# Performance work log

Hardware: AMD Instinct MI355X
Metric: run time of the kernel (lower is better)

The kernel has to match this reference:

```python
import jax, jax.numpy as jnp
import numpy as np

D = 120000   # sample_size
H1 = 600     # sample_size/200
H2 = 300     # sample_size/400
H3 = 200     # sample_size/600
DENSITY = 0.1  # sparselinear default connectivity
B = 512
EPS = 1e-5

_LAYER_SPECS = [(H1, D), (H1, H1), (H2, H1), (H3, H2), (H3, H3)]


def _make_idx(key, out_d, in_d, nnz):
    k1, k2 = jax.random.split(key)
    rows = jax.random.randint(k1, (nnz,), 0, out_d)
    cols = jax.random.randint(k2, (nnz,), 0, in_d)
    return jnp.stack([rows, cols]).astype(jnp.int32)


def setup_inputs() -> dict:
    key = jax.random.key(0)
    ks = jax.random.split(key, 32)
    inp = {"x": jax.random.normal(ks[0], (B, D), jnp.float32)}
    for i, (o, ii) in enumerate(_LAYER_SPECS, 1):
        nnz = int(DENSITY * o * ii)
        scale = 1.0 / np.sqrt(DENSITY * ii)  # kaiming-like fan-in scaling on nonzeros
        inp[f"idx{i}"] = _make_idx(ks[3 * i], o, ii, nnz)
        inp[f"val{i}"] = jax.random.normal(ks[3 * i + 1], (nnz,), jnp.float32) * scale
        inp[f"b{i}"] = jnp.zeros((o,), jnp.float32)
    for j, d in enumerate([H1, H2, H3], 1):
        inp[f"g{j}"] = jnp.ones((d,), jnp.float32)
        inp[f"be{j}"] = jnp.zeros((d,), jnp.float32)
    return inp


def _sp_linear(x, idx, vals, bias, out_d):
    # COO sparse linear: y = x @ W^T + b, W scattered from (row, col, val)
    in_d = x.shape[1]
    W = jnp.zeros((out_d, in_d), x.dtype).at[idx[0], idx[1]].add(vals)
    return x @ W.T + bias


def _bn(x, g, b):
    # BatchNorm1d, training mode: biased batch variance
    m = x.mean(axis=0)
    v = x.var(axis=0)
    return (x - m) * jax.lax.rsqrt(v + EPS) * g + b


def reference(x, idx1, val1, b1, idx2, val2, b2, idx3, val3, b3,
              idx4, val4, b4, idx5, val5, b5,
              g1, be1, g2, be2, g3, be3):
    h = jax.nn.silu(_bn(_sp_linear(x, idx1, val1, b1, H1), g1, be1))
    h = jax.nn.silu(_sp_linear(h, idx2, val2, b2, H1))
    h = jax.nn.silu(_bn(_sp_linear(h, idx3, val3, b3, H2), g2, be2))
    h = jax.nn.silu(_bn(_sp_linear(h, idx4, val4, b4, H3), g3, be3))
    return _sp_linear(h, idx5, val5, b5, H3)
```

## Files before the change

### kernel.cpp

```cpp
#include <hip/hip_runtime.h>

typedef unsigned short ushort_t;
typedef unsigned int uint_t;

typedef __bf16 bf16x8 __attribute__((ext_vector_type(8)));
typedef float  floatx4 __attribute__((ext_vector_type(4)));

#define AS3 __attribute__((address_space(3)))
#define AS1 __attribute__((address_space(1)))

#define BATCH 512
#define D_IN  120000
#define N1P   640
#define N2P   640
#define N3P   320
#define N4P   256
#define N5P   256

#define HALF    60000
#define CHW     15000
#define NREG    1200
#define NB      256
#define RSTRIDE 6912

static constexpr long O_W1 = 0;
static constexpr long SZ_W1 = 640L * 120000 * 2;
static constexpr long O_W2 = O_W1 + SZ_W1;
static constexpr long SZ_W2 = 640L * 640 * 4;
static constexpr long O_W3 = O_W2 + SZ_W2;
static constexpr long SZ_W3 = 320L * 640 * 4;
static constexpr long O_W4 = O_W3 + SZ_W3;
static constexpr long SZ_W4 = 256L * 320 * 4;
static constexpr long O_W5 = O_W4 + SZ_W4;
static constexpr long SZ_W5 = 256L * 256 * 4;
static constexpr long O_Y1 = O_W5 + SZ_W5;
static constexpr long SZ_Y1 = 512L * 640 * 4;
static constexpr long ZERO_OFF = O_W2;
static constexpr long ZERO_BYTES = (O_Y1 + SZ_Y1) - O_W2;
static constexpr long O_XB = O_Y1 + SZ_Y1;
static constexpr long SZ_XB = 512L * 120000 * 2;
static constexpr long O_CNT = O_XB;
static constexpr long O_OFF = O_CNT + (long)NREG * NB * 4;
static constexpr long O_TOT = O_OFF + (long)NB * NREG * 4;
static constexpr long O_REC = O_TOT + 4800;
static constexpr long O_H1 = O_XB;
static constexpr long O_H2 = O_H1 + 512L * 640 * 4;
static constexpr long O_Y3 = O_H2 + 512L * 640 * 4;
static constexpr long O_H3 = O_Y3 + 512L * 320 * 4;
static constexpr long O_Y4 = O_H3 + 512L * 320 * 4;
static constexpr long O_H4 = O_Y4 + 512L * 256 * 4;

__device__ __forceinline__ ushort_t f2bf(float f) {
    union { float f; uint_t u; } x;
    x.f = f;
    uint_t u = x.u;
    return (ushort_t)((u + 0x7FFFu + ((u >> 16) & 1u)) >> 16);
}
__device__ __forceinline__ float silu_f(float z) {
    return z / (1.f + expf(-z));
}
__device__ __forceinline__ void load16_lds(const void* g, void* l) {
    __builtin_amdgcn_global_load_lds((const AS1 char*)g, (AS3 char*)l, 16, 0, 0);
}

__global__ void zero_f4(float4* __restrict__ p, long n4) {
    long stride = (long)gridDim.x * blockDim.x;
    for (long i = (long)blockIdx.x * blockDim.x + threadIdx.x; i < n4; i += stride)
        p[i] = make_float4(0.f, 0.f, 0.f, 0.f);
}

__global__ void cast_f32_bf16(const float* __restrict__ X, ushort_t* __restrict__ Xb, long n8) {
    long t = (long)blockIdx.x * blockDim.x + threadIdx.x;
    if (t >= n8) return;
    const float4* p = (const float4*)X + 2 * t;
    float4 a = p[0], b = p[1];
    union { ushort_t us[8]; uint4 v; } u;
    u.us[0] = f2bf(a.x); u.us[1] = f2bf(a.y); u.us[2] = f2bf(a.z); u.us[3] = f2bf(a.w);
    u.us[4] = f2bf(b.x); u.us[5] = f2bf(b.y); u.us[6] = f2bf(b.z); u.us[7] = f2bf(b.w);
    ((uint4*)Xb)[t] = u.v;
}

__global__ __launch_bounds__(512) void hist1(const int* __restrict__ idx, int nnz, int chunk,
                                             int* __restrict__ counts ) {
    __shared__ uint_t h[NREG];
    const int b = blockIdx.x, t = threadIdx.x;
    for (int i = t; i < NREG; i += 512) h[i] = 0;
    __syncthreads();
    const int s = b * chunk;
    const int e = min(s + chunk, nnz);
    for (int i = s + t; i < e; i += 512) {
        int r = idx[i];
        int c = idx[nnz + i];
        atomicAdd(&h[r * 2 + (c >= HALF ? 1 : 0)], 1u);
    }
    __syncthreads();
    for (int i = t; i < NREG; i += 512) counts[(long)i * NB + b] = (int)h[i];
}

__global__ __launch_bounds__(NB) void scan1(const int* __restrict__ counts ,
                                            int* __restrict__ offs ,
                                            int* __restrict__ totals) {
    __shared__ int s[NB];
    const int reg = blockIdx.x, t = threadIdx.x;
    const int v = counts[(long)reg * NB + t];
    s[t] = v;
    __syncthreads();
    for (int o = 1; o < NB; o <<= 1) {
        int x = (t >= o) ? s[t - o] : 0;
        __syncthreads();
        s[t] += x;
        __syncthreads();
    }
    offs[(long)t * NREG + reg] = s[t] - v;
    if (t == NB - 1) totals[reg] = s[t];
}

__global__ __launch_bounds__(512) void scatter1(const int* __restrict__ idx,
                                                const float* __restrict__ vals,
                                                int nnz, int chunk,
                                                const int* __restrict__ offs ,
                                                int2* __restrict__ rec) {
    __shared__ int cur[NREG];
    const int b = blockIdx.x, t = threadIdx.x;
    const int* ob = offs + (long)b * NREG;
    for (int i = t; i < NREG; i += 512) cur[i] = i * RSTRIDE + ob[i];
    __syncthreads();
    const int s = b * chunk;
    const int e = min(s + chunk, nnz);
    for (int i = s + t; i < e; i += 512) {
        int r = idx[i];
        int c = idx[nnz + i];
        float v = vals[i];
        int h = (c >= HALF) ? 1 : 0;
        int reg = r * 2 + h;
        int slot = atomicAdd(&cur[reg], 1);
        if (slot < (reg + 1) * RSTRIDE)
            rec[slot] = make_int2(c - h * HALF, __float_as_int(v));
    }
}

__global__ __launch_bounds__(512) void build_w1(const int2* __restrict__ rec,
                                                const int* __restrict__ totals,
                                                ushort_t* __restrict__ W) {
    const int bid = blockIdx.x;
    const int r = bid >> 1, h = bid & 1;
    const int t = threadIdx.x;
    ushort_t* dstbase = W + (size_t)r * D_IN + h * HALF;

    if (r >= 600) {
        uint4 z = make_uint4(0, 0, 0, 0);
        for (int j = t * 8; j < HALF; j += 512 * 8) *(uint4*)(dstbase + j) = z;
        return;
    }

    __shared__ int2 lrec[RSTRIDE];
    __shared__ float acc[CHW];

    const int reg = r * 2 + h;
    const int n = min(totals[reg], RSTRIDE);
    const int2* src = rec + (long)reg * RSTRIDE;
    for (int i = t; i < n; i += 512) lrec[i] = src[i];
    __syncthreads();

#pragma unroll
    for (int ch = 0; ch < 4; ch++) {
        for (int j = t * 4; j < CHW; j += 512 * 4)
            *(float4*)&acc[j] = make_float4(0.f, 0.f, 0.f, 0.f);
        __syncthreads();
        const int base = ch * CHW;
        for (int i = t; i < n; i += 512) {
            int2 e = lrec[i];
            unsigned off = (unsigned)(e.x - base);
            if (off < (unsigned)CHW)
                atomicAdd(&acc[off], __int_as_float(e.y));
        }
        __syncthreads();
        ushort_t* dst = dstbase + base;
        for (int j = t * 8; j < CHW; j += 512 * 8) {
            union { ushort_t us[8]; uint4 v; } u;
#pragma unroll
            for (int k = 0; k < 8; k++) u.us[k] = f2bf(acc[j + k]);
            *(uint4*)(dst + j) = u.v;
        }
        __syncthreads();
    }
}

__global__ void scatter_f32(const int* __restrict__ idx, const float* __restrict__ vals,
                            int nnz, float* __restrict__ W, int ldw) {
    int i = blockIdx.x * blockDim.x + threadIdx.x;
    if (i >= nnz) return;
    atomicAdd(&W[(size_t)idx[i] * ldw + idx[nnz + i]], vals[i]);
}

__global__ __launch_bounds__(256) void gemm1(const ushort_t* __restrict__ X,
                                             const ushort_t* __restrict__ W,
                                             float* __restrict__ Y, int kChunk) {
    __shared__ ushort_t sA[128 * 32];
    __shared__ ushort_t sB[128 * 32];

    const int tile = blockIdx.x;
    const int bm = tile / 5, bn = tile % 5;
    const int ks = blockIdx.y * kChunk;
    const int iters = kChunk / 32;

    const int t = threadIdx.x;
    const int lane = t & 63;
    const int w = t >> 6;
    const int wm = w >> 1, wn = w & 1;

    const int c0 = w * 128 + lane;
    const int c1 = c0 + 64;
    const int rA0 = c0 >> 2, qA0 = c0 & 3;
    const int rA1 = c1 >> 2, qA1 = c1 & 3;

    const ushort_t* pa0 = X + (size_t)(bm * 128 + rA0) * D_IN + ks + qA0 * 8;
    const ushort_t* pa1 = X + (size_t)(bm * 128 + rA1) * D_IN + ks + qA1 * 8;
    const ushort_t* pb0 = W + (size_t)(bn * 128 + rA0) * D_IN + ks + qA0 * 8;
    const ushort_t* pb1 = W + (size_t)(bn * 128 + rA1) * D_IN + ks + qA1 * 8;

    ushort_t* la0 = sA + (size_t)(w * 128) * 8;
    ushort_t* la1 = sA + (size_t)(w * 128 + 64) * 8;
    ushort_t* lb0 = sB + (size_t)(w * 128) * 8;
    ushort_t* lb1 = sB + (size_t)(w * 128 + 64) * 8;

    const int i16 = lane & 15;
    const int qk = lane >> 4;
    const bf16x8* ap[4];
    const bf16x8* bp[4];
#pragma unroll
    for (int mi = 0; mi < 4; mi++)
        ap[mi] = (const bf16x8*)&sA[(size_t)(wm * 64 + mi * 16 + i16) * 32 + qk * 8];
#pragma unroll
    for (int ni = 0; ni < 4; ni++)
        bp[ni] = (const bf16x8*)&sB[(size_t)(wn * 64 + ni * 16 + i16) * 32 + qk * 8];

    floatx4 acc[4][4] = {};

    for (int it = 0; it < iters; ++it) {
        __syncthreads();
        load16_lds(pa0, la0);
        load16_lds(pa1, la1);
        load16_lds(pb0, lb0);
        load16_lds(pb1, lb1);
        pa0 += 32; pa1 += 32; pb0 += 32; pb1 += 32;
        __syncthreads();

        bf16x8 af[4], bfr[4];
#pragma unroll
        for (int mi = 0; mi < 4; mi++) af[mi] = *ap[mi];
#pragma unroll
        for (int ni = 0; ni < 4; ni++) bfr[ni] = *bp[ni];
#pragma unroll
        for (int mi = 0; mi < 4; mi++)
#pragma unroll
            for (int ni = 0; ni < 4; ni++)
                acc[mi][ni] = __builtin_amdgcn_mfma_f32_16x16x32_bf16(af[mi], bfr[ni], acc[mi][ni], 0, 0, 0);
    }

#pragma unroll
    for (int mi = 0; mi < 4; mi++) {
#pragma unroll
        for (int ni = 0; ni < 4; ni++) {
#pragma unroll
            for (int r = 0; r < 4; r++) {
                int row = bm * 128 + wm * 64 + mi * 16 + qk * 4 + r;
                int col = bn * 128 + wn * 64 + ni * 16 + i16;
                atomicAdd(&Y[(size_t)row * N1P + col], acc[mi][ni][r]);
            }
        }
    }
}

__global__ void bn_silu(const float* __restrict__ Y, int ld, int realN,
                        const float* __restrict__ g, const float* __restrict__ be,
                        float* __restrict__ H) {
    int j = blockIdx.x;
    int t = threadIdx.x;
    if (j >= realN) {
        for (int b = t; b < BATCH; b += 256) H[(size_t)b * ld + j] = 0.f;
        return;
    }
    float v0 = Y[(size_t)t * ld + j];
    float v1 = Y[(size_t)(t + 256) * ld + j];
    __shared__ float rs[256], rss[256];
    rs[t] = v0 + v1;
    rss[t] = v0 * v0 + v1 * v1;
    __syncthreads();
    for (int o = 128; o > 0; o >>= 1) {
        if (t < o) { rs[t] += rs[t + o]; rss[t] += rss[t + o]; }
        __syncthreads();
    }
    float mean = rs[0] * (1.f / 512.f);
    float var  = rss[0] * (1.f / 512.f) - mean * mean;
    float sc = rsqrtf(var + 1e-5f) * g[j];
    float sh = be[j] - mean * sc;
    H[(size_t)t * ld + j]         = silu_f(v0 * sc + sh);
    H[(size_t)(t + 256) * ld + j] = silu_f(v1 * sc + sh);
}

template <int ACT, int GUARD>
__global__ __launch_bounds__(256) void small_gemm(const float* __restrict__ A, int lda,
                                                  const float* __restrict__ W, int ldw,
                                                  const float* __restrict__ bias, int biasN,
                                                  float* __restrict__ out, int ldo, int outN,
                                                  int K) {
    __shared__ float sA[64][20];
    __shared__ float sB[64][20];
    const int t = threadIdx.x;
    const int m0 = blockIdx.x * 64, n0 = blockIdx.y * 64;
    const int ty = t >> 4, tx = t & 15;
    const int lm = t >> 2, lq = t & 3;
    float acc[4][4] = {};

    for (int kt = 0; kt < K; kt += 16) {
        __syncthreads();
        float4 av = *(const float4*)&A[(size_t)(m0 + lm) * lda + kt + lq * 4];
        float4 wv = *(const float4*)&W[(size_t)(n0 + lm) * ldw + kt + lq * 4];
        sA[lm][lq * 4 + 0] = av.x; sA[lm][lq * 4 + 1] = av.y;
        sA[lm][lq * 4 + 2] = av.z; sA[lm][lq * 4 + 3] = av.w;
        sB[lm][lq * 4 + 0] = wv.x; sB[lm][lq * 4 + 1] = wv.y;
        sB[lm][lq * 4 + 2] = wv.z; sB[lm][lq * 4 + 3] = wv.w;
        __syncthreads();
#pragma unroll
        for (int kg = 0; kg < 4; kg++) {
            float4 a4[4], b4[4];
#pragma unroll
            for (int i = 0; i < 4; i++) a4[i] = *(const float4*)&sA[ty * 4 + i][kg * 4];
#pragma unroll
            for (int j = 0; j < 4; j++) b4[j] = *(const float4*)&sB[tx * 4 + j][kg * 4];
#pragma unroll
            for (int i = 0; i < 4; i++)
#pragma unroll
                for (int j = 0; j < 4; j++)
                    acc[i][j] += a4[i].x * b4[j].x + a4[i].y * b4[j].y +
                                 a4[i].z * b4[j].z + a4[i].w * b4[j].w;
        }
    }

#pragma unroll
    for (int i = 0; i < 4; i++) {
#pragma unroll
        for (int j = 0; j < 4; j++) {
            int row = m0 + ty * 4 + i;
            int col = n0 + tx * 4 + j;
            float v = acc[i][j];
            if (bias != nullptr && col < biasN) v += bias[col];
            if (ACT == 1) v = silu_f(v);
            if (GUARD) {
                if (col < outN) out[(size_t)row * ldo + col] = v;
            } else {
                out[(size_t)row * ldo + col] = v;
            }
        }
    }
}

extern "C" void kernel_launch(void* const* d_in, const int* in_sizes, int n_in,
                              void* d_out, int out_size, void* d_ws, size_t ws_size,
                              hipStream_t stream) {
    const float* x   = (const float*)d_in[0];
    const int* idx1 = (const int*)d_in[1];  const float* val1 = (const float*)d_in[2];
    const int* idx2 = (const int*)d_in[4];  const float* val2 = (const float*)d_in[5];
    const float* b2 = (const float*)d_in[6];
    const int* idx3 = (const int*)d_in[7];  const float* val3 = (const float*)d_in[8];
    const int* idx4 = (const int*)d_in[10]; const float* val4 = (const float*)d_in[11];
    const int* idx5 = (const int*)d_in[13]; const float* val5 = (const float*)d_in[14];
    const float* b5 = (const float*)d_in[15];
    const float* g1 = (const float*)d_in[16]; const float* be1 = (const float*)d_in[17];
    const float* g2 = (const float*)d_in[18]; const float* be2 = (const float*)d_in[19];
    const float* g3 = (const float*)d_in[20]; const float* be3 = (const float*)d_in[21];

    const int nnz1 = in_sizes[1] / 2;
    const int nnz2 = in_sizes[4] / 2;
    const int nnz3 = in_sizes[7] / 2;
    const int nnz4 = in_sizes[10] / 2;
    const int nnz5 = in_sizes[13] / 2;

    char* ws = (char*)d_ws;
    ushort_t* W1 = (ushort_t*)(ws + O_W1);
    float* W2 = (float*)(ws + O_W2);
    float* W3 = (float*)(ws + O_W3);
    float* W4 = (float*)(ws + O_W4);
    float* W5 = (float*)(ws + O_W5);
    float* y1 = (float*)(ws + O_Y1);
    int*   cnt = (int*)(ws + O_CNT);
    int*   off = (int*)(ws + O_OFF);
    int*   tot = (int*)(ws + O_TOT);
    int2*  rec = (int2*)(ws + O_REC);
    ushort_t* Xb = (ushort_t*)(ws + O_XB);
    float* h1 = (float*)(ws + O_H1);
    float* h2 = (float*)(ws + O_H2);
    float* y3 = (float*)(ws + O_Y3);
    float* h3 = (float*)(ws + O_H3);
    float* y4 = (float*)(ws + O_Y4);
    float* h4 = (float*)(ws + O_H4);

    zero_f4<<<dim3((unsigned)(ZERO_BYTES / 16 / 256 + 1)), dim3(256), 0, stream>>>(
        (float4*)(ws + ZERO_OFF), ZERO_BYTES / 16);

    {
        const int chunk = (nnz1 + NB - 1) / NB;
        hist1<<<dim3(NB), dim3(512), 0, stream>>>(idx1, nnz1, chunk, cnt);
        scan1<<<dim3(NREG), dim3(NB), 0, stream>>>(cnt, off, tot);
        scatter1<<<dim3(NB), dim3(512), 0, stream>>>(idx1, val1, nnz1, chunk, off, rec);
        build_w1<<<dim3(640 * 2), dim3(512), 0, stream>>>(rec, tot, W1);
    }

    {
        long n8 = (long)BATCH * D_IN / 8;
        cast_f32_bf16<<<dim3((unsigned)((n8 + 255) / 256)), dim3(256), 0, stream>>>(x, Xb, n8);
    }

    scatter_f32<<<dim3((nnz2 + 255) / 256), dim3(256), 0, stream>>>(idx2, val2, nnz2, W2, 640);
    scatter_f32<<<dim3((nnz3 + 255) / 256), dim3(256), 0, stream>>>(idx3, val3, nnz3, W3, 640);
    scatter_f32<<<dim3((nnz4 + 255) / 256), dim3(256), 0, stream>>>(idx4, val4, nnz4, W4, 320);
    scatter_f32<<<dim3((nnz5 + 255) / 256), dim3(256), 0, stream>>>(idx5, val5, nnz5, W5, 256);

    gemm1<<<dim3(20, 30), dim3(256), 0, stream>>>(Xb, W1, y1, 4000);

    bn_silu<<<dim3(N1P), dim3(256), 0, stream>>>(y1, N1P, 600, g1, be1, h1);

    small_gemm<1, 0><<<dim3(8, N2P / 64), dim3(256), 0, stream>>>(h1, N1P, W2, 640, b2, 600,
                                                                  h2, N2P, N2P, 640);
    small_gemm<0, 0><<<dim3(8, N3P / 64), dim3(256), 0, stream>>>(h2, N2P, W3, 640, nullptr, 0,
                                                                  y3, N3P, N3P, 640);
    bn_silu<<<dim3(N3P), dim3(256), 0, stream>>>(y3, N3P, 300, g2, be2, h3);

    small_gemm<0, 0><<<dim3(8, N4P / 64), dim3(256), 0, stream>>>(h3, N3P, W4, 320, nullptr, 0,
                                                                  y4, N4P, N4P, 320);
    bn_silu<<<dim3(N4P), dim3(256), 0, stream>>>(y4, N4P, 200, g3, be3, h4);

    small_gemm<0, 1><<<dim3(8, N5P / 64), dim3(256), 0, stream>>>(h4, N4P, W5, 256, b5, 200,
                                                                  (float*)d_out, 200, 200, 256);
    (void)n_in; (void)out_size; (void)ws_size;
}
```

Baseline: 1.084 ms.

## Fuse fp32-to-bf16 cast of x into double-buffered, swizzled gemm1 and rework bn_silu

Drops the separate kernel that cast x from fp32 to bf16. gemm1 now loads fp32 x directly, converts it in registers with packed bf16 conversion, and stores it into swizzled LDS. gemm1 also double-buffers its A and B tiles so the next K slice is prefetched while MFMAs run, and the K split goes from 30 to 50 chunks. bn_silu is rewritten to give each block 64 columns with coalesced row loops instead of one strided column per block. The intent is to avoid writing and re-reading the full bf16 copy of x and to hide load latency, at the cost of more register pressure and more atomic partial-sum traffic into y1.

Measured after the change: 1.113 ms. +2.7%, slower.

```diff
diff --git a/kernel.cpp b/kernel.cpp
--- a/kernel.cpp
+++ b/kernel.cpp
@@ -16,6 +16,9 @@
 #define N3P   320
 #define N4P   256
 #define N5P   256
+
+#define KSPLIT 50
+#define KCHUNK 2400
 
 #define HALF    60000
 #define CHW     15000
@@ -37,13 +40,12 @@
 static constexpr long SZ_Y1 = 512L * 640 * 4;
 static constexpr long ZERO_OFF = O_W2;
 static constexpr long ZERO_BYTES = (O_Y1 + SZ_Y1) - O_W2;
-static constexpr long O_XB = O_Y1 + SZ_Y1;
-static constexpr long SZ_XB = 512L * 120000 * 2;
-static constexpr long O_CNT = O_XB;
+static constexpr long O_SCR = O_Y1 + SZ_Y1;
+static constexpr long O_CNT = O_SCR;
 static constexpr long O_OFF = O_CNT + (long)NREG * NB * 4;
 static constexpr long O_TOT = O_OFF + (long)NB * NREG * 4;
 static constexpr long O_REC = O_TOT + 4800;
-static constexpr long O_H1 = O_XB;
+static constexpr long O_H1 = O_SCR;
 static constexpr long O_H2 = O_H1 + 512L * 640 * 4;
 static constexpr long O_Y3 = O_H2 + 512L * 640 * 4;
 static constexpr long O_H3 = O_Y3 + 512L * 320 * 4;
@@ -56,6 +58,11 @@
     uint_t u = x.u;
     return (ushort_t)((u + 0x7FFFu + ((u >> 16) & 1u)) >> 16);
 }
+__device__ __forceinline__ uint_t cvt_pk_bf16(float lo, float hi) {
+    uint_t r;
+    asm("v_cvt_pk_bf16_f32 %0, %1, %2" : "=v"(r) : "v"(lo), "v"(hi));
+    return r;
+}
 __device__ __forceinline__ float silu_f(float z) {
     return z / (1.f + expf(-z));
 }
@@ -67,17 +74,6 @@
     long stride = (long)gridDim.x * blockDim.x;
     for (long i = (long)blockIdx.x * blockDim.x + threadIdx.x; i < n4; i += stride)
         p[i] = make_float4(0.f, 0.f, 0.f, 0.f);
-}
-
-__global__ void cast_f32_bf16(const float* __restrict__ X, ushort_t* __restrict__ Xb, long n8) {
-    long t = (long)blockIdx.x * blockDim.x + threadIdx.x;
-    if (t >= n8) return;
-    const float4* p = (const float4*)X + 2 * t;
-    float4 a = p[0], b = p[1];
-    union { ushort_t us[8]; uint4 v; } u;
-    u.us[0] = f2bf(a.x); u.us[1] = f2bf(a.y); u.us[2] = f2bf(a.z); u.us[3] = f2bf(a.w);
-    u.us[4] = f2bf(b.x); u.us[5] = f2bf(b.y); u.us[6] = f2bf(b.z); u.us[7] = f2bf(b.w);
-    ((uint4*)Xb)[t] = u.v;
 }
 
 __global__ __launch_bounds__(512) void hist1(const int* __restrict__ idx, int nnz, int chunk,
@@ -193,69 +189,105 @@
     atomicAdd(&W[(size_t)idx[i] * ldw + idx[nnz + i]], vals[i]);
 }
 
-__global__ __launch_bounds__(256) void gemm1(const ushort_t* __restrict__ X,
+__global__ __launch_bounds__(256) void gemm1(const float* __restrict__ X,
                                              const ushort_t* __restrict__ W,
-                                             float* __restrict__ Y, int kChunk) {
-    __shared__ ushort_t sA[128 * 32];
-    __shared__ ushort_t sB[128 * 32];
+                                             float* __restrict__ Y) {
+    __shared__ ushort_t sA[2][128 * 32];
+    __shared__ ushort_t sB[2][128 * 32];
 
     const int tile = blockIdx.x;
     const int bm = tile / 5, bn = tile % 5;
-    const int ks = blockIdx.y * kChunk;
-    const int iters = kChunk / 32;
+    const int ks = blockIdx.y * KCHUNK;
+    const int iters = KCHUNK / 32;
 
     const int t = threadIdx.x;
     const int lane = t & 63;
     const int w = t >> 6;
     const int wm = w >> 1, wn = w & 1;
-
-    const int c0 = w * 128 + lane;
-    const int c1 = c0 + 64;
-    const int rA0 = c0 >> 2, qA0 = c0 & 3;
-    const int rA1 = c1 >> 2, qA1 = c1 & 3;
-
-    const ushort_t* pa0 = X + (size_t)(bm * 128 + rA0) * D_IN + ks + qA0 * 8;
-    const ushort_t* pa1 = X + (size_t)(bm * 128 + rA1) * D_IN + ks + qA1 * 8;
-    const ushort_t* pb0 = W + (size_t)(bn * 128 + rA0) * D_IN + ks + qA0 * 8;
-    const ushort_t* pb1 = W + (size_t)(bn * 128 + rA1) * D_IN + ks + qA1 * 8;
-
-    ushort_t* la0 = sA + (size_t)(w * 128) * 8;
-    ushort_t* la1 = sA + (size_t)(w * 128 + 64) * 8;
-    ushort_t* lb0 = sB + (size_t)(w * 128) * 8;
-    ushort_t* lb1 = sB + (size_t)(w * 128 + 64) * 8;
-
     const int i16 = lane & 15;
     const int qk = lane >> 4;
-    const bf16x8* ap[4];
-    const bf16x8* bp[4];
-#pragma unroll
-    for (int mi = 0; mi < 4; mi++)
-        ap[mi] = (const bf16x8*)&sA[(size_t)(wm * 64 + mi * 16 + i16) * 32 + qk * 8];
-#pragma unroll
-    for (int ni = 0; ni < 4; ni++)
-        bp[ni] = (const bf16x8*)&sB[(size_t)(wn * 64 + ni * 16 + i16) * 32 + qk * 8];
+
+    const int row0 = t >> 2;
+    const int kq = (t & 3) ^ ((t >> 3) & 3);
+
+    const float* pa0 = X + (size_t)(bm * 128 + row0) * D_IN + ks + kq * 8;
+    const float* pa1 = pa0 + (size_t)64 * D_IN;
+    const ushort_t* pb0 = W + (size_t)(bn * 128 + row0) * D_IN + ks + kq * 8;
+    const ushort_t* pb1 = pb0 + (size_t)64 * D_IN;
+
+    int aoff[4], boff[4];
+#pragma unroll
+    for (int mi = 0; mi < 4; mi++) {
+        int row = wm * 64 + mi * 16 + i16;
+        aoff[mi] = row * 64 + ((qk ^ ((row >> 1) & 3)) * 16);
+    }
+#pragma unroll
+    for (int ni = 0; ni < 4; ni++) {
+        int row = wn * 64 + ni * 16 + i16;
+        boff[ni] = row * 64 + ((qk ^ ((row >> 1) & 3)) * 16);
+    }
+    const char* sAb = (const char*)sA;
+    const char* sBb = (const char*)sB;
 
     floatx4 acc[4][4] = {};
 
+    {
+        load16_lds(pb0, &sB[0][(w * 64) * 8]);
+        load16_lds(pb1, &sB[0][(256 + w * 64) * 8]);
+        float4 a0 = *(const float4*)pa0;
+        float4 a1 = *(const float4*)(pa0 + 4);
+        float4 a2 = *(const float4*)pa1;
+        float4 a3 = *(const float4*)(pa1 + 4);
+        uint4 u0, u1;
+        u0.x = cvt_pk_bf16(a0.x, a0.y); u0.y = cvt_pk_bf16(a0.z, a0.w);
+        u0.z = cvt_pk_bf16(a1.x, a1.y); u0.w = cvt_pk_bf16(a1.z, a1.w);
+        u1.x = cvt_pk_bf16(a2.x, a2.y); u1.y = cvt_pk_bf16(a2.z, a2.w);
+        u1.z = cvt_pk_bf16(a3.x, a3.y); u1.w = cvt_pk_bf16(a3.z, a3.w);
+        *(uint4*)&sA[0][t * 8] = u0;
+        *(uint4*)&sA[0][(t + 256) * 8] = u1;
+        pa0 += 32; pa1 += 32; pb0 += 32; pb1 += 32;
+    }
+    __syncthreads();
+
+    int cur = 0;
     for (int it = 0; it < iters; ++it) {
-        __syncthreads();
-        load16_lds(pa0, la0);
-        load16_lds(pa1, la1);
-        load16_lds(pb0, lb0);
-        load16_lds(pb1, lb1);
-        pa0 += 32; pa1 += 32; pb0 += 32; pb1 += 32;
-        __syncthreads();
+        const int nxt = cur ^ 1;
+        const bool pf = (it + 1 < iters);
+        float4 a0, a1, a2, a3;
+        if (pf) {
+            load16_lds(pb0, &sB[nxt][(w * 64) * 8]);
+            load16_lds(pb1, &sB[nxt][(256 + w * 64) * 8]);
+            a0 = *(const float4*)pa0;
+            a1 = *(const float4*)(pa0 + 4);
+            a2 = *(const float4*)pa1;
+            a3 = *(const float4*)(pa1 + 4);
+            pa0 += 32; pa1 += 32; pb0 += 32; pb1 += 32;
+        }
 
         bf16x8 af[4], bfr[4];
 #pragma unroll
-        for (int mi = 0; mi < 4; mi++) af[mi] = *ap[mi];
-#pragma unroll
-        for (int ni = 0; ni < 4; ni++) bfr[ni] = *bp[ni];
+        for (int mi = 0; mi < 4; mi++)
+            af[mi] = *(const bf16x8*)(sAb + cur * 8192 + aoff[mi]);
+#pragma unroll
+        for (int ni = 0; ni < 4; ni++)
+            bfr[ni] = *(const bf16x8*)(sBb + cur * 8192 + boff[ni]);
 #pragma unroll
         for (int mi = 0; mi < 4; mi++)
 #pragma unroll
             for (int ni = 0; ni < 4; ni++)
                 acc[mi][ni] = __builtin_amdgcn_mfma_f32_16x16x32_bf16(af[mi], bfr[ni], acc[mi][ni], 0, 0, 0);
+
+        if (pf) {
+            uint4 u0, u1;
+            u0.x = cvt_pk_bf16(a0.x, a0.y); u0.y = cvt_pk_bf16(a0.z, a0.w);
+            u0.z = cvt_pk_bf16(a1.x, a1.y); u0.w = cvt_pk_bf16(a1.z, a1.w);
+            u1.x = cvt_pk_bf16(a2.x, a2.y); u1.y = cvt_pk_bf16(a2.z, a2.w);
+            u1.z = cvt_pk_bf16(a3.x, a3.y); u1.w = cvt_pk_bf16(a3.z, a3.w);
+            *(uint4*)&sA[nxt][t * 8] = u0;
+            *(uint4*)&sA[nxt][(t + 256) * 8] = u1;
+        }
+        __syncthreads();
+        cur = nxt;
     }
 
 #pragma unroll
@@ -272,31 +304,48 @@
     }
 }
 
-__global__ void bn_silu(const float* __restrict__ Y, int ld, int realN,
-                        const float* __restrict__ g, const float* __restrict__ be,
-                        float* __restrict__ H) {
-    int j = blockIdx.x;
-    int t = threadIdx.x;
-    if (j >= realN) {
-        for (int b = t; b < BATCH; b += 256) H[(size_t)b * ld + j] = 0.f;
-        return;
-    }
-    float v0 = Y[(size_t)t * ld + j];
-    float v1 = Y[(size_t)(t + 256) * ld + j];
-    __shared__ float rs[256], rss[256];
-    rs[t] = v0 + v1;
-    rss[t] = v0 * v0 + v1 * v1;
-    __syncthreads();
-    for (int o = 128; o > 0; o >>= 1) {
-        if (t < o) { rs[t] += rs[t + o]; rss[t] += rss[t + o]; }
-        __syncthreads();
-    }
-    float mean = rs[0] * (1.f / 512.f);
-    float var  = rss[0] * (1.f / 512.f) - mean * mean;
-    float sc = rsqrtf(var + 1e-5f) * g[j];
-    float sh = be[j] - mean * sc;
-    H[(size_t)t * ld + j]         = silu_f(v0 * sc + sh);
-    H[(size_t)(t + 256) * ld + j] = silu_f(v1 * sc + sh);
+__global__ __launch_bounds__(512) void bn_silu(const float* __restrict__ Y, int ld, int realN,
+                                               const float* __restrict__ g,
+                                               const float* __restrict__ be,
+                                               float* __restrict__ H) {
+    const int t = threadIdx.x;
+    const int sub = t >> 6;
+    const int c = t & 63;
+    const int col = blockIdx.x * 64 + c;
+
+    float s = 0.f, ss = 0.f;
+#pragma unroll 8
+    for (int r = sub; r < BATCH; r += 8) {
+        float v = Y[(size_t)r * ld + col];
+        s += v;
+        ss += v * v;
+    }
+    __shared__ float rs[8][64], rq[8][64], scs[64], shs[64];
+    rs[sub][c] = s;
+    rq[sub][c] = ss;
+    __syncthreads();
+    if (t < 64) {
+        float S = 0.f, SS = 0.f;
+#pragma unroll
+        for (int k = 0; k < 8; k++) { S += rs[k][t]; SS += rq[k][t]; }
+        float mean = S * (1.f / 512.f);
+        float var  = SS * (1.f / 512.f) - mean * mean;
+        int cc = blockIdx.x * 64 + t;
+        float sc = 0.f, sh = 0.f;
+        if (cc < realN) {
+            sc = rsqrtf(var + 1e-5f) * g[cc];
+            sh = be[cc] - mean * sc;
+        }
+        scs[t] = sc;
+        shs[t] = sh;
+    }
+    __syncthreads();
+    const float sc = scs[c], sh = shs[c];
+#pragma unroll 8
+    for (int r = sub; r < BATCH; r += 8) {
+        float v = Y[(size_t)r * ld + col];
+        H[(size_t)r * ld + col] = silu_f(v * sc + sh);
+    }
 }
 
 template <int ACT, int GUARD>
@@ -388,7 +437,6 @@
     int*   off = (int*)(ws + O_OFF);
     int*   tot = (int*)(ws + O_TOT);
     int2*  rec = (int2*)(ws + O_REC);
-    ushort_t* Xb = (ushort_t*)(ws + O_XB);
     float* h1 = (float*)(ws + O_H1);
     float* h2 = (float*)(ws + O_H2);
     float* y3 = (float*)(ws + O_Y3);
@@ -407,29 +455,24 @@
         build_w1<<<dim3(640 * 2), dim3(512), 0, stream>>>(rec, tot, W1);
     }
 
-    {
-        long n8 = (long)BATCH * D_IN / 8;
-        cast_f32_bf16<<<dim3((unsigned)((n8 + 255) / 256)), dim3(256), 0, stream>>>(x, Xb, n8);
-    }
-
     scatter_f32<<<dim3((nnz2 + 255) / 256), dim3(256), 0, stream>>>(idx2, val2, nnz2, W2, 640);
     scatter_f32<<<dim3((nnz3 + 255) / 256), dim3(256), 0, stream>>>(idx3, val3, nnz3, W3, 640);
     scatter_f32<<<dim3((nnz4 + 255) / 256), dim3(256), 0, stream>>>(idx4, val4, nnz4, W4, 320);
     scatter_f32<<<dim3((nnz5 + 255) / 256), dim3(256), 0, stream>>>(idx5, val5, nnz5, W5, 256);
 
-    gemm1<<<dim3(20, 30), dim3(256), 0, stream>>>(Xb, W1, y1, 4000);
-
-    bn_silu<<<dim3(N1P), dim3(256), 0, stream>>>(y1, N1P, 600, g1, be1, h1);
+    gemm1<<<dim3(20, KSPLIT), dim3(256), 0, stream>>>(x, W1, y1);
+
+    bn_silu<<<dim3(N1P / 64), dim3(512), 0, stream>>>(y1, N1P, 600, g1, be1, h1);
 
     small_gemm<1, 0><<<dim3(8, N2P / 64), dim3(256), 0, stream>>>(h1, N1P, W2, 640, b2, 600,
                                                                   h2, N2P, N2P, 640);
     small_gemm<0, 0><<<dim3(8, N3P / 64), dim3(256), 0, stream>>>(h2, N2P, W3, 640, nullptr, 0,
                                                                   y3, N3P, N3P, 640);
-    bn_silu<<<dim3(N3P), dim3(256), 0, stream>>>(y3, N3P, 300, g2, be2, h3);
+    bn_silu<<<dim3(N3P / 64), dim3(512), 0, stream>>>(y3, N3P, 300, g2, be2, h3);
 
     small_gemm<0, 0><<<dim3(8, N4P / 64), dim3(256), 0, stream>>>(h3, N3P, W4, 320, nullptr, 0,
                                                                   y4, N4P, N4P, 320);
-    bn_silu<<<dim3(N4P), dim3(256), 0, stream>>>(y4, N4P, 200, g3, be3, h4);
+    bn_silu<<<dim3(N4P / 64), dim3(512), 0, stream>>>(y4, N4P, 200, g3, be3, h4);
 
     small_gemm<0, 1><<<dim3(8, N5P / 64), dim3(256), 0, stream>>>(h4, N4P, W5, 256, b5, 200,
                                                                   (float*)d_out, 200, 200, 256);
```
